# Optimization experiments

Measured on AMD Instinct MI355X. Metric: run time of the kernel, lower is better.

The kernel has to match this reference:

```python
import jax, jax.numpy as jnp
import numpy as np

N_QUBITS = 14
N_LAYERS = 2
BATCH = 512


def _apply_ry(state, theta, wire):
    # state: [B, 2,...,2] (n_qubits axes of size 2); theta: [B] per-sample angle
    c = jnp.cos(theta * 0.5)[:, None]
    s = jnp.sin(theta * 0.5)[:, None]
    st = jnp.moveaxis(state, wire + 1, 1)
    shp = st.shape
    st = st.reshape(shp[0], 2, -1)
    a0, a1 = st[:, 0], st[:, 1]
    # RY = [[cos, -sin], [sin, cos]] (real matrix, so the state stays real)
    st = jnp.stack([c * a0 - s * a1, s * a0 + c * a1], axis=1)
    return jnp.moveaxis(st.reshape(shp), 1, wire + 1)


def _apply_cnot(state, ctrl, tgt):
    ca, ta = ctrl + 1, tgt + 1
    s0 = jnp.take(state, 0, axis=ca)
    s1 = jnp.take(state, 1, axis=ca)
    # flip target axis on the control=1 slice (axis index shifts if it was after ctrl)
    s1 = jnp.flip(s1, axis=ta if ta < ca else ta - 1)
    return jnp.stack([s0, s1], axis=ca)


def _circuit(x, weights):
    B, n = x.shape
    L = weights.shape[0]
    # |0...0> initial state, batched
    state = jnp.zeros((B,) + (2,) * n, x.dtype).at[(slice(None),) + (0,) * n].set(1.0)
    # angle encoding: RY(x[b, w]) on wire w
    for w in range(n):
        state = _apply_ry(state, x[:, w], w)
    # BasicEntanglerLayers: per layer, RY(weights[l, w]) on each wire, then CNOT ring
    for l in range(L):
        for w in range(n):
            state = _apply_ry(state, jnp.broadcast_to(weights[l, w], (B,)), w)
        for w in range(n):
            state = _apply_cnot(state, w, (w + 1) % n)
    # <Z_w> = P(bit_w = 0) - P(bit_w = 1)
    probs = state * state
    exps = []
    for w in range(n):
        p = jnp.moveaxis(probs, w + 1, 1).reshape(B, 2, -1).sum(-1)
        exps.append(p[:, 0] - p[:, 1])
    return jnp.stack(exps, axis=1)  # [B, n_qubits]


def setup_inputs() -> dict:
    key = jax.random.key(0)
    k1, k2 = jax.random.split(key)
    x = jax.random.normal(k1, (BATCH, N_QUBITS), dtype=jnp.float32)
    weights = (2.0 * np.pi) * jax.random.uniform(k2, (N_LAYERS, N_QUBITS), dtype=jnp.float32)
    return {"x": x, "weights": weights}


def reference(x, weights):
    return _circuit(x, weights)
```

## Files before the change

kernel.cpp:

```cpp
#include <hip/hip_runtime.h>

#define NQ 14
#define BLOCK 256
#define NG 28

typedef float f32x2 __attribute__((ext_vector_type(2)));
__device__ __forceinline__ f32x2 mk2(float a, float b) { f32x2 r; r.x = a; r.y = b; return r; }

struct Sched { unsigned m[NG]; unsigned r[NG]; unsigned fr[NQ]; };

constexpr Sched build_sched() {
  Sched sc{};
  unsigned col[NQ] = {}, rowinv[NQ] = {};
  for (int p = 0; p < NQ; ++p) { col[p] = 1u << p; rowinv[p] = 1u << p; }
  int g = 0;
  for (int l = 0; l < 2; ++l) {
    for (int w = 0; w < NQ; ++w) { int p = NQ - 1 - w; sc.m[g] = col[p]; sc.r[g] = rowinv[p]; ++g; }
    for (int w = 0; w < NQ; ++w) {
      int tgt = (w + 1) % NQ; int pc = NQ - 1 - w, pt = NQ - 1 - tgt;
      col[pc] ^= col[pt]; rowinv[pt] ^= rowinv[pc];
    }
  }
  for (int w = 0; w < NQ; ++w) sc.fr[w] = rowinv[NQ - 1 - w];
  return sc;
}
constexpr Sched SC = build_sched();

constexpr int QA_G[10] = {0, 1, 2, 3, 4, 5, 15, 16, 17, 18};
constexpr int QB_G[10] = {6, 7, 8, 9, 10, 19, 20, 21, 22, 23};
constexpr int QC_G[8]  = {11, 12, 13, 14, 24, 25, 26, 27};

constexpr unsigned lmapA(unsigned v) { return (v >> 8) & 63u; }
constexpr unsigned lmapB(unsigned v) { return ((v >> 8) & 1u) | (((v >> 3) & 31u) << 1); }
constexpr unsigned lmapC(unsigned v) { return (v & 0xFu) | ((v >> 8) & 0x30u); }

constexpr bool sched_ok() {
  const unsigned spanA = 0x3F00u, spanB = 0x01F8u, spanC = 0x300Fu;
  for (int k = 0; k < 10; ++k) {
    if (SC.m[QA_G[k]] & ~spanA) return false;
    if (!(__builtin_popcount(lmapA(SC.m[QA_G[k]]) & lmapA(SC.r[QA_G[k]])) & 1)) return false;
  }
  for (int k = 0; k < 10; ++k) {
    if (SC.m[QB_G[k]] & ~spanB) return false;
    if (!(__builtin_popcount(lmapB(SC.m[QB_G[k]]) & lmapB(SC.r[QB_G[k]])) & 1)) return false;
  }
  for (int k = 0; k < 8; ++k) {
    if (SC.m[QC_G[k]] & ~spanC) return false;
    if (!(__builtin_popcount(lmapC(SC.m[QC_G[k]]) & lmapC(SC.r[QC_G[k]])) & 1)) return false;
  }
  int ord[NG] = {}; int n = 0;
  for (int k = 0; k < 10; ++k) ord[n++] = QA_G[k];
  for (int k = 0; k < 10; ++k) ord[n++] = QB_G[k];
  for (int k = 0; k < 8;  ++k) ord[n++] = QC_G[k];
  for (int g = 0; g < NG; ++g) { int c = 0; for (int i = 0; i < NG; ++i) if (ord[i] == g) ++c; if (c != 1) return false; }
  for (int i = 0; i < NG; ++i)
    for (int j = i + 1; j < NG; ++j)
      if (ord[i] > ord[j]) {
        int a = ord[i], b = ord[j];
        if ((__builtin_popcount(SC.r[a] & SC.m[b]) & 1) != (__builtin_popcount(SC.r[b] & SC.m[a]) & 1)) return false;
      }
  return true;
}
static_assert(sched_ok(), "schedule invalid");

constexpr unsigned iQA(unsigned t, unsigned p, unsigned e) { return t | ((2u * p + e) << 8); }
constexpr unsigned iQB(unsigned t, unsigned p, unsigned e) { return (t & 7u) | (p << 3) | (e << 8) | ((t >> 3) << 9); }
constexpr unsigned iQC(unsigned T, unsigned p, unsigned e) {
  return e | ((p & 7u) << 1) | (((p >> 3) & 3u) << 12) | (((T >> 3) & 15u) << 4) | (((T >> 7) & 1u) << 8) | ((T & 7u) << 9);
}

constexpr unsigned a1s(unsigned i) { unsigned tA = i & 255u, lA = i >> 8; return tA * 64u + (lA ^ ((tA & 15u) << 1)); }
constexpr unsigned Tof(unsigned i)  { return ((i >> 9) & 7u) | (((i >> 4) & 15u) << 3) | (((i >> 8) & 1u) << 7); }
constexpr unsigned lCof(unsigned i) { return (i & 15u) | (((i >> 12) & 3u) << 4); }
constexpr unsigned a2s(unsigned i) { unsigned T = Tof(i), l = lCof(i); return T * 64u + (l ^ ((T & 7u) << 2)); }

__host__ __device__ constexpr unsigned f2_QAw(unsigned t, unsigned p) {
  return 32u * t + (p ^ (t & 15u));
}
__host__ __device__ constexpr unsigned f2_QBr(unsigned t, unsigned p) {
  return 256u * p + 32u * (t & 7u) + (((t >> 3) ^ (t & 7u)) ^ (8u * (p & 1u)));
}
__host__ __device__ constexpr unsigned dw_QBw(unsigned t, unsigned p, unsigned e) {
  const unsigned lc = (t & 7u) | (8u * (p & 1u)) | (16u * ((t >> 6) & 3u));
  return 64u * ((t >> 3) & 7u) + 512u * (p >> 1) + 8192u * e + (lc ^ (((t >> 3) & 7u) << 2));
}
__host__ __device__ constexpr unsigned f2_QCr(unsigned t, unsigned p) {
  return 32u * t + (p ^ ((t & 7u) << 1));
}

constexpr bool basis_ok() {
  for (int mapi = 0; mapi < 3; ++mapi) {
    unsigned acc = 0;
    for (int k = 0; k < 14; ++k) {
      unsigned t = 0, p = 0, e = 0;
      if (k < 8) t = 1u << k; else if (k < 13) p = 1u << (k - 8); else e = 1;
      unsigned v = (mapi == 0) ? iQA(t, p, e) : (mapi == 1) ? iQB(t, p, e) : iQC(t, p, e);
      if (__builtin_popcount(v) != 1 || (acc & v)) return false;
      acc |= v;
    }
    if (acc != 0x3FFFu) return false;
  }
  return true;
}
static_assert(basis_ok(), "layout maps not bijective");

constexpr bool chk_addr(int pat, unsigned t0, unsigned t1) {
  for (unsigned t = t0; t < t1; ++t)
    for (unsigned p = 0; p < 32; ++p)
      for (unsigned e = 0; e < 2; ++e) {
        unsigned a = 0, b = 0;
        if (pat == 0) { a = 2u * f2_QAw(t, p) + e; b = a1s(iQA(t, p, e)); }
        if (pat == 1) { a = 2u * f2_QBr(t, p) + e; b = a1s(iQB(t, p, e)); }
        if (pat == 2) { a = dw_QBw(t, p, e);       b = a2s(iQB(t, p, e)); }
        if (pat == 3) { a = 2u * f2_QCr(t, p) + e; b = a2s(iQC(t, p, e)); }
        if (a != b || a >= 16384u) return false;
      }
  return true;
}
static_assert(chk_addr(0, 0, 128) && chk_addr(0, 128, 256), "QA write addr");
static_assert(chk_addr(1, 0, 128) && chk_addr(1, 128, 256), "QB read addr");
static_assert(chk_addr(2, 0, 128) && chk_addr(2, 128, 256), "QB write addr");
static_assert(chk_addr(3, 0, 128) && chk_addr(3, 128, 256), "QC read addr");

template <unsigned MU, unsigned RHO>
__device__ __forceinline__ void gate_pk(f32x2* v, const float cg, const float sb) {
  const f32x2 C = mk2(cg, cg);
  constexpr unsigned M2 = MU >> 1;
  constexpr bool ODD = (MU & 1u) != 0;
  if constexpr (!ODD) {
    constexpr unsigned LSB = M2 & (0u - M2);
#pragma unroll
    for (unsigned p = 0; p < 32; ++p) {
      if (p & LSB) continue;
      const unsigned q = p ^ M2;
      const int s0 = __builtin_popcount((2u * p) & RHO) & 1;
      const int s1 = __builtin_popcount((2u * p + 1u) & RHO) & 1;
      const f32x2 Sp = mk2(s0 ? -sb : sb, s1 ? -sb : sb);
      const f32x2 Xp = v[p], Xq = v[q];
      v[p] = C * Xp - Sp * Xq;
      v[q] = C * Xq + Sp * Xp;
    }
  } else if constexpr (M2 == 0) {
#pragma unroll
    for (unsigned p = 0; p < 32; ++p) {
      const int s0 = __builtin_popcount((2u * p) & RHO) & 1;
      const f32x2 Sp = mk2(s0 ? -sb : sb, s0 ? sb : -sb);
      const f32x2 X = v[p];
      v[p] = C * X - Sp * mk2(X.y, X.x);
    }
  } else {
    constexpr unsigned LSB = M2 & (0u - M2);
#pragma unroll
    for (unsigned p = 0; p < 32; ++p) {
      if (p & LSB) continue;
      const unsigned q = p ^ M2;
      const int s0 = __builtin_popcount((2u * p) & RHO) & 1;
      const int s1 = __builtin_popcount((2u * p + 1u) & RHO) & 1;
      const f32x2 Sp = mk2(s0 ? -sb : sb, s1 ? -sb : sb);
      const f32x2 Xp = v[p], Xq = v[q];
      const f32x2 T = Sp * Xp;
      v[p] = C * Xp - Sp * mk2(Xq.y, Xq.x);
      v[q] = C * Xq + mk2(T.y, T.x);
    }
  }
}

__global__ __launch_bounds__(BLOCK, 2) void qnn_kernel(
    const float* __restrict__ x, const float* __restrict__ wts,
    float* __restrict__ out) {
  __shared__ float S[16384];
  f32x2* const F = (f32x2*)S;
  const unsigned t = threadIdx.x;
  const int b = blockIdx.x;

  f32x2 v2[32];

  {
    float cxx[NQ], sxx[NQ];
#pragma unroll
    for (int w = 0; w < NQ; ++w) __sincosf(0.5f * x[b * NQ + w], &sxx[w], &cxx[w]);
    float pl = 1.0f;
#pragma unroll
    for (int bb = 0; bb < 8; ++bb) pl *= ((t >> bb) & 1) ? sxx[13 - bb] : cxx[13 - bb];
    v2[0] = mk2(pl * cxx[5], pl * sxx[5]);
#pragma unroll
    for (int k = 1; k < 6; ++k) {
      const unsigned K = 1u << (k - 1);
      const f32x2 sk = mk2(sxx[5 - k], sxx[5 - k]);
      const f32x2 ck = mk2(cxx[5 - k], cxx[5 - k]);
#pragma unroll
      for (unsigned p = 0; p < 16; ++p) {
        if (p & ~(K - 1u)) continue;
        v2[p | K] = v2[p] * sk;
        v2[p] = v2[p] * ck;
      }
    }
  }

#define RUN_GATE(LM, G, BASEPAR)                                          \
  {                                                                       \
    float sn, cs;                                                         \
    __sincosf(0.5f * wts[G], &sn, &cs);                                   \
    const float sb =                                                      \
        (__builtin_popcount((BASEPAR) & SC.r[G]) & 1) ? -sn : sn;         \
    gate_pk<LM(SC.m[G]), LM(SC.r[G])>(v2, cs, sb);                        \
  }

  {
    const unsigned base = t;
    RUN_GATE(lmapA, QA_G[0], base) RUN_GATE(lmapA, QA_G[1], base)
    RUN_GATE(lmapA, QA_G[2], base) RUN_GATE(lmapA, QA_G[3], base)
    RUN_GATE(lmapA, QA_G[4], base) RUN_GATE(lmapA, QA_G[5], base)
    RUN_GATE(lmapA, QA_G[6], base) RUN_GATE(lmapA, QA_G[7], base)
    RUN_GATE(lmapA, QA_G[8], base) RUN_GATE(lmapA, QA_G[9], base)
#pragma unroll
    for (unsigned p = 0; p < 32; ++p) F[f2_QAw(t, p)] = v2[p];
  }
  __syncthreads();

  {
    const unsigned base = (t & 7u) | ((t >> 3) << 9);
#pragma unroll
    for (unsigned p = 0; p < 32; ++p) v2[p] = F[f2_QBr(t, p)];
    RUN_GATE(lmapB, QB_G[0], base) RUN_GATE(lmapB, QB_G[1], base)
    RUN_GATE(lmapB, QB_G[2], base) RUN_GATE(lmapB, QB_G[3], base)
    RUN_GATE(lmapB, QB_G[4], base) RUN_GATE(lmapB, QB_G[5], base)
    RUN_GATE(lmapB, QB_G[6], base) RUN_GATE(lmapB, QB_G[7], base)
    RUN_GATE(lmapB, QB_G[8], base) RUN_GATE(lmapB, QB_G[9], base)
  }
  __syncthreads();
  {
#pragma unroll
    for (unsigned p = 0; p < 32; ++p) {
      S[dw_QBw(t, p, 0)] = v2[p].x;
      S[dw_QBw(t, p, 1)] = v2[p].y;
    }
  }
  __syncthreads();

  float ex[NQ];
  {
    const unsigned base = (((t >> 3) & 15u) << 4) | (((t >> 7) & 1u) << 8) | ((t & 7u) << 9);
#pragma unroll
    for (unsigned p = 0; p < 32; ++p) v2[p] = F[f2_QCr(t, p)];
    RUN_GATE(lmapC, QC_G[0], base) RUN_GATE(lmapC, QC_G[1], base)
    RUN_GATE(lmapC, QC_G[2], base) RUN_GATE(lmapC, QC_G[3], base)
    RUN_GATE(lmapC, QC_G[4], base) RUN_GATE(lmapC, QC_G[5], base)
    RUN_GATE(lmapC, QC_G[6], base) RUN_GATE(lmapC, QC_G[7], base)

#pragma unroll
    for (unsigned p = 0; p < 32; ++p) v2[p] = v2[p] * v2[p];
#pragma unroll
    for (int k = 0; k < 5; ++k) {
      const unsigned K = 1u << k;
#pragma unroll
      for (unsigned p = 0; p < 32; ++p) {
        if (p & K) continue;
        const f32x2 A = v2[p], B = v2[p ^ K];
        v2[p] = A + B;
        v2[p ^ K] = A - B;
      }
    }
#pragma unroll
    for (int w = 0; w < NQ; ++w) {
      const unsigned ls = lmapC(SC.fr[w]);
      const f32x2 W = v2[ls >> 1];
      const float coef = (ls & 1u) ? (W.x - W.y) : (W.x + W.y);
      const int tf = __builtin_popcount(base & SC.fr[w]) & 1;
      ex[w] = tf ? -coef : coef;
    }
  }
  __syncthreads();

#pragma unroll
  for (int w = 0; w < NQ; ++w) {
#pragma unroll
    for (int off = 32; off > 0; off >>= 1) ex[w] += __shfl_xor(ex[w], off, 64);
  }
  const unsigned lane = t & 63u, wave = t >> 6;
  if (lane == 0) {
#pragma unroll
    for (int w = 0; w < NQ; ++w) S[wave * NQ + w] = ex[w];
  }
  __syncthreads();
  if (t < NQ) {
    out[b * NQ + t] = S[t] + S[NQ + t] + S[2 * NQ + t] + S[3 * NQ + t];
  }
#undef RUN_GATE
}

extern "C" void kernel_launch(void* const* d_in, const int* in_sizes, int n_in,
                              void* d_out, int out_size, void* d_ws, size_t ws_size,
                              hipStream_t stream) {
  const float* x = (const float*)d_in[0];
  const float* weights = (const float*)d_in[1];
  float* out = (float*)d_out;
  const int B = in_sizes[0] / NQ;
  qnn_kernel<<<B, BLOCK, 0, stream>>>(x, weights, out);
}
```

Measured before the change: 65.33 us.

## Fold first-layer weight rotations into angle-encoding RY angles

After: 63.44 us. 2.9% less time.

```diff
diff --git a/kernel.cpp b/kernel.cpp
--- a/kernel.cpp
+++ b/kernel.cpp
@@ -26,35 +26,37 @@
 }
 constexpr Sched SC = build_sched();
 
-constexpr int QA_G[10] = {0, 1, 2, 3, 4, 5, 15, 16, 17, 18};
-constexpr int QB_G[10] = {6, 7, 8, 9, 10, 19, 20, 21, 22, 23};
-constexpr int QC_G[8]  = {11, 12, 13, 14, 24, 25, 26, 27};
+constexpr int QA_G[4] = {15, 16, 17, 18};
+constexpr int QB_G[5] = {19, 20, 21, 22, 23};
+constexpr int QC_G[5] = {14, 24, 25, 26, 27};
 
 constexpr unsigned lmapA(unsigned v) { return (v >> 8) & 63u; }
 constexpr unsigned lmapB(unsigned v) { return ((v >> 8) & 1u) | (((v >> 3) & 31u) << 1); }
 constexpr unsigned lmapC(unsigned v) { return (v & 0xFu) | ((v >> 8) & 0x30u); }
 
 constexpr bool sched_ok() {
+  for (int g = 0; g < 14; ++g)
+    if (SC.m[g] != (1u << (13 - g)) || SC.r[g] != (1u << (13 - g))) return false;
   const unsigned spanA = 0x3F00u, spanB = 0x01F8u, spanC = 0x300Fu;
-  for (int k = 0; k < 10; ++k) {
+  for (int k = 0; k < 4; ++k) {
     if (SC.m[QA_G[k]] & ~spanA) return false;
     if (!(__builtin_popcount(lmapA(SC.m[QA_G[k]]) & lmapA(SC.r[QA_G[k]])) & 1)) return false;
   }
-  for (int k = 0; k < 10; ++k) {
+  for (int k = 0; k < 5; ++k) {
     if (SC.m[QB_G[k]] & ~spanB) return false;
     if (!(__builtin_popcount(lmapB(SC.m[QB_G[k]]) & lmapB(SC.r[QB_G[k]])) & 1)) return false;
   }
-  for (int k = 0; k < 8; ++k) {
+  for (int k = 0; k < 5; ++k) {
     if (SC.m[QC_G[k]] & ~spanC) return false;
     if (!(__builtin_popcount(lmapC(SC.m[QC_G[k]]) & lmapC(SC.r[QC_G[k]])) & 1)) return false;
   }
-  int ord[NG] = {}; int n = 0;
-  for (int k = 0; k < 10; ++k) ord[n++] = QA_G[k];
-  for (int k = 0; k < 10; ++k) ord[n++] = QB_G[k];
-  for (int k = 0; k < 8;  ++k) ord[n++] = QC_G[k];
-  for (int g = 0; g < NG; ++g) { int c = 0; for (int i = 0; i < NG; ++i) if (ord[i] == g) ++c; if (c != 1) return false; }
-  for (int i = 0; i < NG; ++i)
-    for (int j = i + 1; j < NG; ++j)
+  int ord[14] = {}; int n = 0;
+  for (int k = 0; k < 4; ++k) ord[n++] = QA_G[k];
+  for (int k = 0; k < 5; ++k) ord[n++] = QB_G[k];
+  for (int k = 0; k < 5; ++k) ord[n++] = QC_G[k];
+  for (int g = 14; g < NG; ++g) { int c = 0; for (int i = 0; i < 14; ++i) if (ord[i] == g) ++c; if (c != 1) return false; }
+  for (int i = 0; i < 14; ++i)
+    for (int j = i + 1; j < 14; ++j)
       if (ord[i] > ord[j]) {
         int a = ord[i], b = ord[j];
         if ((__builtin_popcount(SC.r[a] & SC.m[b]) & 1) != (__builtin_popcount(SC.r[b] & SC.m[a]) & 1)) return false;
@@ -170,7 +172,7 @@
     float* __restrict__ out) {
   __shared__ float S[16384];
   f32x2* const F = (f32x2*)S;
-  const unsigned t = threadIdx.x;
+  const unsigned t = threadIdx.x & 255u;
   const int b = blockIdx.x;
 
   f32x2 v2[32];
@@ -178,7 +180,8 @@
   {
     float cxx[NQ], sxx[NQ];
 #pragma unroll
-    for (int w = 0; w < NQ; ++w) __sincosf(0.5f * x[b * NQ + w], &sxx[w], &cxx[w]);
+    for (int w = 0; w < NQ; ++w)
+      __sincosf(0.5f * (x[b * NQ + w] + wts[w]), &sxx[w], &cxx[w]);
     float pl = 1.0f;
 #pragma unroll
     for (int bb = 0; bb < 8; ++bb) pl *= ((t >> bb) & 1) ? sxx[13 - bb] : cxx[13 - bb];
@@ -210,9 +213,6 @@
     const unsigned base = t;
     RUN_GATE(lmapA, QA_G[0], base) RUN_GATE(lmapA, QA_G[1], base)
     RUN_GATE(lmapA, QA_G[2], base) RUN_GATE(lmapA, QA_G[3], base)
-    RUN_GATE(lmapA, QA_G[4], base) RUN_GATE(lmapA, QA_G[5], base)
-    RUN_GATE(lmapA, QA_G[6], base) RUN_GATE(lmapA, QA_G[7], base)
-    RUN_GATE(lmapA, QA_G[8], base) RUN_GATE(lmapA, QA_G[9], base)
 #pragma unroll
     for (unsigned p = 0; p < 32; ++p) F[f2_QAw(t, p)] = v2[p];
   }
@@ -224,9 +224,7 @@
     for (unsigned p = 0; p < 32; ++p) v2[p] = F[f2_QBr(t, p)];
     RUN_GATE(lmapB, QB_G[0], base) RUN_GATE(lmapB, QB_G[1], base)
     RUN_GATE(lmapB, QB_G[2], base) RUN_GATE(lmapB, QB_G[3], base)
-    RUN_GATE(lmapB, QB_G[4], base) RUN_GATE(lmapB, QB_G[5], base)
-    RUN_GATE(lmapB, QB_G[6], base) RUN_GATE(lmapB, QB_G[7], base)
-    RUN_GATE(lmapB, QB_G[8], base) RUN_GATE(lmapB, QB_G[9], base)
+    RUN_GATE(lmapB, QB_G[4], base)
   }
   __syncthreads();
   {
@@ -245,8 +243,7 @@
     for (unsigned p = 0; p < 32; ++p) v2[p] = F[f2_QCr(t, p)];
     RUN_GATE(lmapC, QC_G[0], base) RUN_GATE(lmapC, QC_G[1], base)
     RUN_GATE(lmapC, QC_G[2], base) RUN_GATE(lmapC, QC_G[3], base)
-    RUN_GATE(lmapC, QC_G[4], base) RUN_GATE(lmapC, QC_G[5], base)
-    RUN_GATE(lmapC, QC_G[6], base) RUN_GATE(lmapC, QC_G[7], base)
+    RUN_GATE(lmapC, QC_G[4], base)
 
 #pragma unroll
     for (unsigned p = 0; p < 32; ++p) v2[p] = v2[p] * v2[p];
```
